# Performance work log

Hardware: AMD Instinct MI355X
Metric: run time of the kernel (lower is better)

Reference implementation:

```python
import jax, jax.numpy as jnp
import numpy as np

B, C_IN, C_OUT, H, W = 4, 256, 256, 56, 56
NH, K, P = 2, 5, 2
HD = C_OUT // NH          # 128
SE_H = C_OUT // 16        # 16
SE_H2 = max(SE_H // 16, 1)  # 1
EPS = 1e-5


def setup_inputs() -> dict:
    key = jax.random.key(0)
    ks = jax.random.split(key, 16)
    n = lambda k, sh, s=1.0: jax.random.normal(k, sh, jnp.float32) * s

    def bn_params(k, c):
        k1, k2 = jax.random.split(k)
        return (1.0 + 0.1 * n(k1, (c,)), 0.1 * n(k2, (c,)),
                jnp.zeros((c,), jnp.float32), jnp.ones((c,), jnp.float32))

    agg_g1, agg_b1, agg_m1, agg_v1 = bn_params(ks[6], C_OUT)
    agg_g2, agg_b2, agg_m2, agg_v2 = bn_params(ks[7], C_OUT)
    se_g_in, se_b_in, se_m_in, se_v_in = bn_params(ks[8], SE_H)
    se_g_out, se_b_out, se_m_out, se_v_out = bn_params(ks[9], C_OUT)
    return {
        "x": n(ks[0], (B, C_IN, H, W)),
        "Wq": n(ks[1], (C_OUT, C_IN), C_IN ** -0.5),
        "Wk": n(ks[2], (C_OUT, C_IN), C_IN ** -0.5),
        "Wv": n(ks[3], (C_OUT, C_IN), C_IN ** -0.5),
        "rel_h": n(ks[4], (HD, 1, 1, K, 1)),
        "rel_w": n(ks[5], (HD, 1, 1, 1, K)),
        "agg_g1": agg_g1, "agg_b1": agg_b1, "agg_m1": agg_m1, "agg_v1": agg_v1,
        "agg_W": n(ks[10], (C_OUT, C_OUT), C_OUT ** -0.5),
        "agg_g2": agg_g2, "agg_b2": agg_b2, "agg_m2": agg_m2, "agg_v2": agg_v2,
        "se_Win": n(ks[11], (SE_H, C_OUT), C_OUT ** -0.5),
        "se_g_in": se_g_in, "se_b_in": se_b_in, "se_m_in": se_m_in, "se_v_in": se_v_in,
        "se_fc1": n(ks[12], (SE_H2, SE_H), SE_H ** -0.5),
        "se_fc2": n(ks[13], (SE_H, SE_H2)),
        "se_Wout": n(ks[14], (C_OUT, SE_H), SE_H ** -0.5),
        "se_g_out": se_g_out, "se_b_out": se_b_out, "se_m_out": se_m_out, "se_v_out": se_v_out,
    }


def _conv1x1(Wm, t):
    return jnp.einsum('oc,bchw->bohw', Wm, t)


def _bn(t, g, b, m, v):
    # eval-mode BatchNorm2d with running stats
    return (t - m[:, None, None]) * (g * jax.lax.rsqrt(v + EPS))[:, None, None] + b[:, None, None]


def _windows(t):
    # (B, O, H+2P, W+2P) -> (B, O, H, W, K, K), matching torch unfold(2,K,1).unfold(3,K,1)
    w = jnp.stack([t[:, :, i:i + H, j:j + W] for i in range(K) for j in range(K)], axis=-1)
    return w.reshape(t.shape[0], t.shape[1], H, W, K, K)


def reference(x, Wq, Wk, Wv, rel_h, rel_w,
              agg_g1, agg_b1, agg_m1, agg_v1, agg_W, agg_g2, agg_b2, agg_m2, agg_v2,
              se_Win, se_g_in, se_b_in, se_m_in, se_v_in, se_fc1, se_fc2, se_Wout,
              se_g_out, se_b_out, se_m_out, se_v_out):
    xp = jnp.pad(x, ((0, 0), (0, 0), (P, P), (P, P)))
    q = _conv1x1(Wq, x).reshape(B, NH, HD, H, W)          # (B,NH,HD,H,W)
    k_win = _windows(_conv1x1(Wk, xp))                    # (B,O,H,W,K,K)
    v_win = _windows(_conv1x1(Wv, xp))
    # relative position bias: first head gets rel_h (height taps), second gets rel_w
    k_win = jnp.concatenate([k_win[:, :HD] + rel_h[None], k_win[:, HD:] + rel_w[None]], axis=1)
    k_r = k_win.reshape(B, NH, HD, H, W, K * K)
    v_r = v_win.reshape(B, NH, HD, H, W, K * K)
    scores = jnp.einsum('bnchw,bnchwk->bnhwk', q, k_r) / jnp.sqrt(jnp.float32(HD))
    attn = jax.nn.softmax(scores, axis=-1)
    out = jnp.einsum('bnhwk,bnchwk->bnchw', attn, v_r).reshape(B, C_OUT, H, W)
    # agg: BN -> ReLU -> 1x1 conv -> BN
    y = jax.nn.relu(_bn(out, agg_g1, agg_b1, agg_m1, agg_v1))
    y = _bn(_conv1x1(agg_W, y), agg_g2, agg_b2, agg_m2, agg_v2)
    # squeeze-excitation (intended math; original view(b,c) is a channel-count bug)
    s = jax.nn.relu(_bn(_conv1x1(se_Win, y), se_g_in, se_b_in, se_m_in, se_v_in))  # (B,SE_H,H,W)
    p = s.mean(axis=(2, 3))                                                        # (B,SE_H)
    g = jax.nn.sigmoid(jax.nn.relu(p @ se_fc1.T) @ se_fc2.T)                       # (B,SE_H)
    s = s * g[:, :, None, None]
    return _bn(_conv1x1(se_Wout, s), se_g_out, se_b_out, se_m_out, se_v_out)
```

## Files before the change

kernel.cpp:

```cpp
#include <hip/hip_runtime.h>
#include <hip/hip_bf16.h>

#define HW 3136
#define HH 56
#define WW 56
#define BB 4
#define CC 256
#define HD 128

#define TH 2
#define TW 8
#define WR 6
#define WC 12
#define WPX 72
#define KSTR2 136
#define RSTR 132

#define ASTR 72

typedef __attribute__((ext_vector_type(8))) short bf16x8;
typedef __attribute__((ext_vector_type(4))) float f32x4;

__device__ __forceinline__ unsigned short f2bf(float f) {
    unsigned int u; __builtin_memcpy(&u, &f, 4);
    unsigned int r = u + 0x7FFFu + ((u >> 16) & 1u);
    return (unsigned short)(r >> 16);
}
__device__ __forceinline__ float bflo(unsigned int u) {
    unsigned int x = u << 16; float f; __builtin_memcpy(&f, &x, 4); return f;
}
__device__ __forceinline__ float bfhi(unsigned int u) {
    unsigned int x = u & 0xFFFF0000u; float f; __builtin_memcpy(&f, &x, 4); return f;
}

__global__ __launch_bounds__(256) void xt_cvt(const float* __restrict__ x,
                                              unsigned short* __restrict__ xt)
{
    int b = blockIdx.z;
    int c0 = blockIdx.y * 64;
    int p0 = blockIdx.x * 64;
    __shared__ float tile[64][65];
    int t = threadIdx.x;
    int p4 = t & 15, cl = t >> 4;
    const float* xb = x + ((size_t)b * CC + c0) * HW + p0;
#pragma unroll
    for (int i = 0; i < 4; i++) {
        int c = cl + 16 * i;
        float4 f = *(const float4*)(xb + (size_t)c * HW + p4 * 4);
        tile[c][p4 * 4 + 0] = f.x; tile[c][p4 * 4 + 1] = f.y;
        tile[c][p4 * 4 + 2] = f.z; tile[c][p4 * 4 + 3] = f.w;
    }
    __syncthreads();
    int c2 = t & 31, pl = t >> 5;
    unsigned short* xo = xt + ((size_t)b * HW + p0) * CC + c0;
#pragma unroll
    for (int i = 0; i < 8; i++) {
        int p = pl + 8 * i;
        float a = tile[2 * c2][p], bb = tile[2 * c2 + 1][p];
        unsigned int pk = (unsigned int)f2bf(a) | ((unsigned int)f2bf(bb) << 16);
        *(unsigned int*)(xo + (size_t)p * CC + 2 * c2) = pk;
    }
}

__global__ __launch_bounds__(256) void wcvt(const float* __restrict__ Wq,
                                            const float* __restrict__ Wk,
                                            const float* __restrict__ Wv,
                                            const float* __restrict__ Wa,
                                            const float* __restrict__ Wse,
                                            unsigned short* __restrict__ wb,
                                            float* __restrict__ psum)
{
    int t = threadIdx.x;
    if (blockIdx.y == 4) {
        if (blockIdx.x == 0 && t < 64) psum[t] = 0.f;
        int idx = blockIdx.x * 256 + t;
        if (idx < 1024) {
            float4 f = *(const float4*)(Wse + (size_t)idx * 4);
            uint2 pk;
            pk.x = (unsigned int)f2bf(f.x) | ((unsigned int)f2bf(f.y) << 16);
            pk.y = (unsigned int)f2bf(f.z) | ((unsigned int)f2bf(f.w) << 16);
            *(uint2*)(wb + (size_t)4 * 65536 + (size_t)idx * 4) = pk;
        }
        return;
    }
    const float* srcs[4] = {Wq, Wk, Wv, Wa};
    const float* s = srcs[blockIdx.y];
    int idx = blockIdx.x * 256 + t;
    float4 f = *(const float4*)(s + (size_t)idx * 4);
    uint2 pk;
    pk.x = (unsigned int)f2bf(f.x) | ((unsigned int)f2bf(f.y) << 16);
    pk.y = (unsigned int)f2bf(f.z) | ((unsigned int)f2bf(f.w) << 16);
    *(uint2*)(wb + (size_t)blockIdx.y * 65536 + (size_t)idx * 4) = pk;
}

__global__ __launch_bounds__(256) void qkv_mfma(
    const unsigned short* __restrict__ xt, const unsigned short* __restrict__ wqkv,
    unsigned short* __restrict__ q_ws, unsigned short* __restrict__ k_ws,
    unsigned short* __restrict__ v_ws)
{
    int wsel = blockIdx.z;
    unsigned short* outp = (wsel == 0) ? q_ws : ((wsel == 1) ? k_ws : v_ws);
    int gp0 = blockIdx.x * 128, o0 = blockIdx.y * 128;

    __shared__ unsigned short As[128 * ASTR];
    __shared__ unsigned short Bs[128 * ASTR];
    const unsigned short* xb = xt + (size_t)gp0 * CC;
    const unsigned short* wbp = wqkv + (size_t)wsel * 65536 + (size_t)o0 * CC;

    int t = threadIdx.x;
    int wave = t >> 6, lane = t & 63;
    int mo = (wave & 1) * 64, no = (wave >> 1) * 64;
    int lm = lane & 15, lq = lane >> 4;
    int sr = t >> 3, sc = t & 7;

    f32x4 acc[4][4];
#pragma unroll
    for (int i = 0; i < 4; i++)
#pragma unroll
        for (int j = 0; j < 4; j++) acc[i][j] = (f32x4){0.f, 0.f, 0.f, 0.f};

    for (int k0 = 0; k0 < 256; k0 += 64) {
#pragma unroll
        for (int i = 0; i < 4; i++) {
            int r = sr + 32 * i;
            *(uint4*)&As[r * ASTR + sc * 8] = *(const uint4*)(xb + (size_t)r * CC + k0 + sc * 8);
            *(uint4*)&Bs[r * ASTR + sc * 8] = *(const uint4*)(wbp + (size_t)r * CC + k0 + sc * 8);
        }
        __syncthreads();
#pragma unroll
        for (int ks = 0; ks < 64; ks += 32) {
            bf16x8 af[4], bfr[4];
#pragma unroll
            for (int i = 0; i < 4; i++)
                af[i] = *(bf16x8*)&As[(mo + 16 * i + lm) * ASTR + ks + lq * 8];
#pragma unroll
            for (int j = 0; j < 4; j++)
                bfr[j] = *(bf16x8*)&Bs[(no + 16 * j + lm) * ASTR + ks + lq * 8];
#pragma unroll
            for (int i = 0; i < 4; i++)
#pragma unroll
                for (int j = 0; j < 4; j++)
                    acc[i][j] = __builtin_amdgcn_mfma_f32_16x16x32_bf16(
                        af[i], bfr[j], acc[i][j], 0, 0, 0);
        }
        __syncthreads();
    }
    unsigned short* ob = outp + (size_t)gp0 * CC + o0;
    bool ev = (lm & 1) == 0;
    int elm = lm & ~1;
#pragma unroll
    for (int i = 0; i < 4; i++)
#pragma unroll
        for (int j = 0; j < 4; j++)
#pragma unroll
            for (int r = 0; r < 4; r++) {
                float v = acc[i][j][r];
                float p = __shfl_xor(v, 1, 64);
                unsigned int pk = ev
                    ? ((unsigned int)f2bf(v) | ((unsigned int)f2bf(p) << 16))
                    : ((unsigned int)f2bf(p) | ((unsigned int)f2bf(v) << 16));
                if (ev == (r < 2)) {
                    int m = mo + 16 * i + lq * 4 + r;
                    int n = no + 16 * j + elm;
                    *(unsigned int*)(ob + (size_t)m * CC + n) = pk;
                }
            }
}

__global__ __launch_bounds__(256) void agg_mfma(
    const unsigned short* __restrict__ ao, const unsigned short* __restrict__ wagg,
    const float* __restrict__ g1, const float* __restrict__ b1,
    const float* __restrict__ m1, const float* __restrict__ v1,
    const float* __restrict__ g2, const float* __restrict__ b2,
    const float* __restrict__ m2, const float* __restrict__ v2,
    float* __restrict__ y2)
{
    int gp0 = blockIdx.x * 128, o0 = blockIdx.y * 128;

    __shared__ unsigned short As[128 * ASTR];
    __shared__ unsigned short Bs[128 * ASTR];
    __shared__ float s1[256], o1[256], s2[256], o2[256];

    int t = threadIdx.x;
    {
        float sc1 = g1[t] * rsqrtf(v1[t] + 1e-5f);
        s1[t] = sc1; o1[t] = b1[t] - m1[t] * sc1;
        float sc2 = g2[t] * rsqrtf(v2[t] + 1e-5f);
        s2[t] = sc2; o2[t] = b2[t] - m2[t] * sc2;
    }

    const unsigned short* aob = ao + (size_t)gp0 * CC;
    const unsigned short* wbp = wagg + (size_t)o0 * CC;

    int wave = t >> 6, lane = t & 63;
    int mo = (wave & 1) * 64, no = (wave >> 1) * 64;
    int lm = lane & 15, lq = lane >> 4;
    int sr = t >> 3, sc = t & 7;

    f32x4 acc[4][4];
#pragma unroll
    for (int i = 0; i < 4; i++)
#pragma unroll
        for (int j = 0; j < 4; j++) acc[i][j] = (f32x4){0.f, 0.f, 0.f, 0.f};

    __syncthreads();

    for (int k0 = 0; k0 < 256; k0 += 64) {
#pragma unroll
        for (int i = 0; i < 4; i++) {
            int r = sr + 32 * i;
            int cb = k0 + sc * 8;
            uint4 u = *(const uint4*)(aob + (size_t)r * CC + cb);
            float e[8] = {bflo(u.x), bfhi(u.x), bflo(u.y), bfhi(u.y),
                          bflo(u.z), bfhi(u.z), bflo(u.w), bfhi(u.w)};
            unsigned short pk[8];
#pragma unroll
            for (int uu = 0; uu < 8; uu++) {
                float vv = fmaxf(e[uu] * s1[cb + uu] + o1[cb + uu], 0.f);
                pk[uu] = f2bf(vv);
            }
            *(uint4*)&As[r * ASTR + sc * 8] = *(uint4*)pk;
            *(uint4*)&Bs[r * ASTR + sc * 8] = *(const uint4*)(wbp + (size_t)r * CC + k0 + sc * 8);
        }
        __syncthreads();
#pragma unroll
        for (int ks = 0; ks < 64; ks += 32) {
            bf16x8 af[4], bfr[4];
#pragma unroll
            for (int i = 0; i < 4; i++)
                af[i] = *(bf16x8*)&As[(mo + 16 * i + lm) * ASTR + ks + lq * 8];
#pragma unroll
            for (int j = 0; j < 4; j++)
                bfr[j] = *(bf16x8*)&Bs[(no + 16 * j + lm) * ASTR + ks + lq * 8];
#pragma unroll
            for (int i = 0; i < 4; i++)
#pragma unroll
                for (int j = 0; j < 4; j++)
                    acc[i][j] = __builtin_amdgcn_mfma_f32_16x16x32_bf16(
                        af[i], bfr[j], acc[i][j], 0, 0, 0);
        }
        __syncthreads();
    }
    float* yb = y2 + (size_t)gp0 * CC + o0;
#pragma unroll
    for (int i = 0; i < 4; i++)
#pragma unroll
        for (int j = 0; j < 4; j++)
#pragma unroll
            for (int r = 0; r < 4; r++) {
                int m = mo + 16 * i + lq * 4 + r;
                int n = no + 16 * j + lm;
                yb[(size_t)m * CC + n] = acc[i][j][r] * s2[o0 + n] + o2[o0 + n];
            }
}

__global__ __launch_bounds__(256) void attn_kernel(
    const unsigned short* __restrict__ q_ws, const unsigned short* __restrict__ k_ws,
    const unsigned short* __restrict__ v_ws,
    const float* __restrict__ rel_h, const float* __restrict__ rel_w,
    unsigned short* __restrict__ ao_ws)
{
    __shared__ unsigned short kwin[WPX * KSTR2];
    __shared__ float relT[5 * RSTR];

    int t = threadIdx.x;
    int tile = blockIdx.x;
    int n = blockIdx.y;
    int b = blockIdx.z;
    int tr = tile / 7, tc = tile - tr * 7;
    int h0 = tr * TH, w0 = tc * TW;
    const float* rel = (n == 0) ? rel_h : rel_w;
    const size_t base = (size_t)b * HW * CC + n * HD;

    {
        int c16 = t & 15, pwt = t >> 4;
#pragma unroll
        for (int it = 0; it < 5; it++) {
            int pw = pwt + it * 16;
            if (pw < WPX) {
                int wr = pw / 12, wc = pw - wr * 12;
                int gh = h0 + wr - 2, gw = w0 + wc - 2;
                uint4 u = make_uint4(0u, 0u, 0u, 0u);
                if (gh >= 0 && gh < HH && gw >= 0 && gw < WW)
                    u = *(const uint4*)(k_ws + base + (size_t)(gh * WW + gw) * CC + c16 * 8);
                *(uint4*)&kwin[pw * KSTR2 + c16 * 8] = u;
            }
        }
        if (t < 128) {
#pragma unroll
            for (int tt = 0; tt < 5; tt++)
                relT[tt * RSTR + t] = rel[t * 5 + tt];
        }
    }
    __syncthreads();

    int px = t >> 4, cg = t & 15;
    int pr = px >> 3, pc = px & 7;
    int ghp = h0 + pr, gwp = w0 + pc;
    const size_t pbase = base + (size_t)(ghp * WW + gwp) * CC;

    float q[8];
    {
        uint4 uq = *(const uint4*)(q_ws + pbase + cg * 8);
        q[0] = bflo(uq.x); q[1] = bfhi(uq.x); q[2] = bflo(uq.y); q[3] = bfhi(uq.y);
        q[4] = bflo(uq.z); q[5] = bfhi(uq.z); q[6] = bflo(uq.w); q[7] = bfhi(uq.w);
    }

    float acc[30];
#pragma unroll
    for (int tt = 0; tt < 25; tt++) {
        int di = tt / 5, dj = tt - 5 * (tt / 5);
        int wpx = (pr + di) * WC + pc + dj;
        uint4 ku = *(const uint4*)&kwin[wpx * KSTR2 + cg * 8];
        acc[tt] = q[0] * bflo(ku.x) + q[1] * bfhi(ku.x)
                + q[2] * bflo(ku.y) + q[3] * bfhi(ku.y)
                + q[4] * bflo(ku.z) + q[5] * bfhi(ku.z)
                + q[6] * bflo(ku.w) + q[7] * bfhi(ku.w);
    }
#pragma unroll
    for (int tt = 0; tt < 5; tt++) {
        float4 r0 = *(const float4*)&relT[tt * RSTR + cg * 8];
        float4 r1 = *(const float4*)&relT[tt * RSTR + cg * 8 + 4];
        acc[25 + tt] = q[0] * r0.x + q[1] * r0.y + q[2] * r0.z + q[3] * r0.w
                     + q[4] * r1.x + q[5] * r1.y + q[6] * r1.z + q[7] * r1.w;
    }
#pragma unroll
    for (int tt = 0; tt < 30; tt++) {
#pragma unroll
        for (int m = 1; m < 16; m <<= 1)
            acc[tt] += __shfl_xor(acc[tt], m, 64);
    }
    {
        const float inv = 0.08838834764831845f;
        float mx = -1e30f;
#pragma unroll
        for (int tt = 0; tt < 25; tt++) {
            int di = tt / 5, dj = tt - 5 * (tt / 5);
            acc[tt] = (acc[tt] + ((n == 0) ? acc[25 + di] : acc[25 + dj])) * inv;
            mx = fmaxf(mx, acc[tt]);
        }
        float sum = 0.f;
#pragma unroll
        for (int tt = 0; tt < 25; tt++) { acc[tt] = __expf(acc[tt] - mx); sum += acc[tt]; }
        float rs = 1.f / sum;
#pragma unroll
        for (int tt = 0; tt < 25; tt++) acc[tt] *= rs;
    }
    __syncthreads();

    {
        int c16 = t & 15, pwt = t >> 4;
#pragma unroll
        for (int it = 0; it < 5; it++) {
            int pw = pwt + it * 16;
            if (pw < WPX) {
                int wr = pw / 12, wc = pw - wr * 12;
                int gh = h0 + wr - 2, gw = w0 + wc - 2;
                uint4 u = make_uint4(0u, 0u, 0u, 0u);
                if (gh >= 0 && gh < HH && gw >= 0 && gw < WW)
                    u = *(const uint4*)(v_ws + base + (size_t)(gh * WW + gw) * CC + c16 * 8);
                *(uint4*)&kwin[pw * KSTR2 + c16 * 8] = u;
            }
        }
    }
    __syncthreads();

    float o[8];
#pragma unroll
    for (int i = 0; i < 8; i++) o[i] = 0.f;
#pragma unroll
    for (int tt = 0; tt < 25; tt++) {
        int di = tt / 5, dj = tt - 5 * (tt / 5);
        int wpx = (pr + di) * WC + pc + dj;
        float a = acc[tt];
        uint4 vu = *(const uint4*)&kwin[wpx * KSTR2 + cg * 8];
        o[0] += a * bflo(vu.x); o[1] += a * bfhi(vu.x);
        o[2] += a * bflo(vu.y); o[3] += a * bfhi(vu.y);
        o[4] += a * bflo(vu.z); o[5] += a * bfhi(vu.z);
        o[6] += a * bflo(vu.w); o[7] += a * bfhi(vu.w);
    }
    uint4 pk;
    pk.x = (unsigned int)f2bf(o[0]) | ((unsigned int)f2bf(o[1]) << 16);
    pk.y = (unsigned int)f2bf(o[2]) | ((unsigned int)f2bf(o[3]) << 16);
    pk.z = (unsigned int)f2bf(o[4]) | ((unsigned int)f2bf(o[5]) << 16);
    pk.w = (unsigned int)f2bf(o[6]) | ((unsigned int)f2bf(o[7]) << 16);
    *(uint4*)(ao_ws + pbase + cg * 8) = pk;
}

__global__ __launch_bounds__(256) void se_in_mfma(
    const float* __restrict__ y2, const unsigned short* __restrict__ wse,
    const float* __restrict__ gin, const float* __restrict__ bin,
    const float* __restrict__ min_, const float* __restrict__ vin,
    float* __restrict__ s_ws, float* __restrict__ psum)
{
    int wave = threadIdx.x >> 6, lane = threadIdx.x & 63;
    int tile = blockIdx.x * 4 + wave;
    int gp0 = tile * 16;
    int b = tile / 196;
    int lm = lane & 15, lq = lane >> 4;

    f32x4 acc = (f32x4){0.f, 0.f, 0.f, 0.f};
    const float* ya = y2 + (size_t)(gp0 + lm) * CC;
#pragma unroll
    for (int k0 = 0; k0 < 256; k0 += 32) {
        int kb = k0 + lq * 8;
        float4 f0 = *(const float4*)(ya + kb);
        float4 f1 = *(const float4*)(ya + kb + 4);
        unsigned short pk[8] = {f2bf(f0.x), f2bf(f0.y), f2bf(f0.z), f2bf(f0.w),
                                f2bf(f1.x), f2bf(f1.y), f2bf(f1.z), f2bf(f1.w)};
        bf16x8 af = *(bf16x8*)pk;
        bf16x8 bf = *(const bf16x8*)(wse + (size_t)lm * CC + kb);
        acc = __builtin_amdgcn_mfma_f32_16x16x32_bf16(af, bf, acc, 0, 0, 0);
    }
    float sc = gin[lm] * rsqrtf(vin[lm] + 1e-5f);
    float off = bin[lm] - min_[lm] * sc;
    float sum4 = 0.f;
#pragma unroll
    for (int r = 0; r < 4; r++) {
        int row = lq * 4 + r;
        float v = fmaxf(acc[r] * sc + off, 0.f);
        s_ws[(size_t)(gp0 + row) * 16 + lm] = v;
        sum4 += v;
    }
    sum4 += __shfl_xor(sum4, 16, 64);
    sum4 += __shfl_xor(sum4, 32, 64);
    if (lane < 16) atomicAdd(&psum[b * 16 + lane], sum4);
}

__global__ __launch_bounds__(256) void se_out_kernel(
    const float* __restrict__ s_ws, const float* __restrict__ psum,
    const float* __restrict__ fc1, const float* __restrict__ fc2,
    const float* __restrict__ se_Wout,
    const float* __restrict__ gout, const float* __restrict__ bout,
    const float* __restrict__ mout, const float* __restrict__ vout,
    float* __restrict__ out)
{
    int b = blockIdx.y;
    int px0 = blockIdx.x * 32;
    __shared__ float sl[32 * 17];
    __shared__ float wg[256 * 20];
    __shared__ float bo[256];
    __shared__ float gg[16];
    int t = threadIdx.x;

    if (t < 16) {
        float h = 0.f;
#pragma unroll
        for (int jj = 0; jj < 16; jj++)
            h += (psum[b * 16 + jj] * (1.f / 3136.f)) * fc1[jj];
        h = fmaxf(h, 0.f);
        float z = h * fc2[t];
        gg[t] = 1.f / (1.f + __expf(-z));
    }
    {
        const float* sb = s_ws + (size_t)(b * HW + px0) * 16;
#pragma unroll
        for (int i = 0; i < 2; i++) {
            int idx = t + 256 * i;
            sl[(idx >> 4) * 17 + (idx & 15)] = sb[idx];
        }
    }
    __syncthreads();
    {
        float sc = gout[t] * rsqrtf(vout[t] + 1e-5f);
        bo[t] = bout[t] - mout[t] * sc;
        const float* wr = se_Wout + (size_t)t * 16;
#pragma unroll
        for (int k = 0; k < 16; k++)
            wg[t * 20 + k] = wr[k] * gg[k] * sc;
    }
    __syncthreads();

    int px = t & 31, og = t >> 5;
    float4 s0 = *(float4*)&sl[px * 17 + 0];
    float4 s1v = *(float4*)&sl[px * 17 + 4];
    float4 s2v = *(float4*)&sl[px * 17 + 8];
    float4 s3 = *(float4*)&sl[px * 17 + 12];
    float* ob = out + (size_t)b * CC * HW + px0 + px;
#pragma unroll
    for (int oi = 0; oi < 32; oi++) {
        int o = og * 32 + oi;
        float4 w0 = *(float4*)&wg[o * 20 + 0];
        float4 w1 = *(float4*)&wg[o * 20 + 4];
        float4 w2 = *(float4*)&wg[o * 20 + 8];
        float4 w3 = *(float4*)&wg[o * 20 + 12];
        float r = bo[o]
            + s0.x * w0.x + s0.y * w0.y + s0.z * w0.z + s0.w * w0.w
            + s1v.x * w1.x + s1v.y * w1.y + s1v.z * w1.z + s1v.w * w1.w
            + s2v.x * w2.x + s2v.y * w2.y + s2v.z * w2.z + s2v.w * w2.w
            + s3.x * w3.x + s3.y * w3.y + s3.z * w3.z + s3.w * w3.w;
        ob[(size_t)o * HW] = r;
    }
}

extern "C" void kernel_launch(void* const* d_in, const int* in_sizes, int n_in,
                              void* d_out, int out_size, void* d_ws, size_t ws_size,
                              hipStream_t stream) {
    const float* x     = (const float*)d_in[0];
    const float* Wq    = (const float*)d_in[1];
    const float* Wk    = (const float*)d_in[2];
    const float* Wv    = (const float*)d_in[3];
    const float* rel_h = (const float*)d_in[4];
    const float* rel_w = (const float*)d_in[5];
    const float* agg_g1 = (const float*)d_in[6];
    const float* agg_b1 = (const float*)d_in[7];
    const float* agg_m1 = (const float*)d_in[8];
    const float* agg_v1 = (const float*)d_in[9];
    const float* agg_W  = (const float*)d_in[10];
    const float* agg_g2 = (const float*)d_in[11];
    const float* agg_b2 = (const float*)d_in[12];
    const float* agg_m2 = (const float*)d_in[13];
    const float* agg_v2 = (const float*)d_in[14];
    const float* se_Win = (const float*)d_in[15];
    const float* se_g_in = (const float*)d_in[16];
    const float* se_b_in = (const float*)d_in[17];
    const float* se_m_in = (const float*)d_in[18];
    const float* se_v_in = (const float*)d_in[19];
    const float* se_fc1  = (const float*)d_in[20];
    const float* se_fc2  = (const float*)d_in[21];
    const float* se_Wout = (const float*)d_in[22];
    const float* se_g_out = (const float*)d_in[23];
    const float* se_b_out = (const float*)d_in[24];
    const float* se_m_out = (const float*)d_in[25];
    const float* se_v_out = (const float*)d_in[26];

    const size_t NQ = (size_t)BB * HW * CC;
    unsigned short* q_ws  = (unsigned short*)d_ws;
    unsigned short* k_ws  = q_ws + NQ;
    unsigned short* v_ws  = k_ws + NQ;
    unsigned short* ao_ws = v_ws + NQ;
    unsigned short* xt    = ao_ws;
    float* y2_ws = (float*)d_ws;
    float* s_ws  = (float*)(ao_ws + NQ);
    float* psum  = s_ws + (size_t)BB * HW * 16;
    unsigned short* wbf = (unsigned short*)(psum + 64);

    xt_cvt<<<dim3(49, 4, 4), 256, 0, stream>>>(x, xt);
    wcvt<<<dim3(64, 5), 256, 0, stream>>>(Wq, Wk, Wv, agg_W, se_Win, wbf, psum);
    qkv_mfma<<<dim3(98, 2, 3), 256, 0, stream>>>(xt, wbf, q_ws, k_ws, v_ws);
    attn_kernel<<<dim3(196, 2, 4), 256, 0, stream>>>(q_ws, k_ws, v_ws, rel_h, rel_w, ao_ws);
    agg_mfma<<<dim3(98, 2), 256, 0, stream>>>(ao_ws, wbf + 3 * 65536,
        agg_g1, agg_b1, agg_m1, agg_v1, agg_g2, agg_b2, agg_m2, agg_v2, y2_ws);
    se_in_mfma<<<dim3(196), 256, 0, stream>>>(y2_ws, wbf + 4 * 65536,
        se_g_in, se_b_in, se_m_in, se_v_in, s_ws, psum);
    se_out_kernel<<<dim3(98, 4), 256, 0, stream>>>(s_ws, psum, se_fc1, se_fc2,
        se_Wout, se_g_out, se_b_out, se_m_out, se_v_out, (float*)d_out);
}
```

Measured before the change: 199.6 us.

## Drop LDS staging in attention kernel and merge prep conversion kernels

The attention kernel no longer stages a 6x12 K/V halo window in shared memory behind barriers. Each thread now reads its 25 K and V neighbours straight from global memory, relying on L1/L2 for reuse across the 16 row-contiguous pixels in a block, and reads the relative-position bias directly as well. The x transpose/convert and weight-convert kernels are merged into one launch to save a kernel launch. The risk is more global/cache traffic and less explicit reuse in attention, in exchange for removing LDS writes, syncs and the shared-memory footprint.

```diff
diff --git a/kernel.cpp b/kernel.cpp
--- a/kernel.cpp
+++ b/kernel.cpp
@@ -8,14 +8,6 @@
 #define CC 256
 #define HD 128
 
-#define TH 2
-#define TW 8
-#define WR 6
-#define WC 12
-#define WPX 72
-#define KSTR2 136
-#define RSTR 132
-
 #define ASTR 72
 
 typedef __attribute__((ext_vector_type(8))) short bf16x8;
@@ -33,36 +25,9 @@
     unsigned int x = u & 0xFFFF0000u; float f; __builtin_memcpy(&f, &x, 4); return f;
 }
 
-__global__ __launch_bounds__(256) void xt_cvt(const float* __restrict__ x,
-                                              unsigned short* __restrict__ xt)
-{
-    int b = blockIdx.z;
-    int c0 = blockIdx.y * 64;
-    int p0 = blockIdx.x * 64;
-    __shared__ float tile[64][65];
-    int t = threadIdx.x;
-    int p4 = t & 15, cl = t >> 4;
-    const float* xb = x + ((size_t)b * CC + c0) * HW + p0;
-#pragma unroll
-    for (int i = 0; i < 4; i++) {
-        int c = cl + 16 * i;
-        float4 f = *(const float4*)(xb + (size_t)c * HW + p4 * 4);
-        tile[c][p4 * 4 + 0] = f.x; tile[c][p4 * 4 + 1] = f.y;
-        tile[c][p4 * 4 + 2] = f.z; tile[c][p4 * 4 + 3] = f.w;
-    }
-    __syncthreads();
-    int c2 = t & 31, pl = t >> 5;
-    unsigned short* xo = xt + ((size_t)b * HW + p0) * CC + c0;
-#pragma unroll
-    for (int i = 0; i < 8; i++) {
-        int p = pl + 8 * i;
-        float a = tile[2 * c2][p], bb = tile[2 * c2 + 1][p];
-        unsigned int pk = (unsigned int)f2bf(a) | ((unsigned int)f2bf(bb) << 16);
-        *(unsigned int*)(xo + (size_t)p * CC + 2 * c2) = pk;
-    }
-}
-
-__global__ __launch_bounds__(256) void wcvt(const float* __restrict__ Wq,
+__global__ __launch_bounds__(256) void prep(const float* __restrict__ x,
+                                            unsigned short* __restrict__ xt,
+                                            const float* __restrict__ Wq,
                                             const float* __restrict__ Wk,
                                             const float* __restrict__ Wv,
                                             const float* __restrict__ Wa,
@@ -70,27 +35,57 @@
                                             unsigned short* __restrict__ wb,
                                             float* __restrict__ psum)
 {
+    int bid = blockIdx.x;
     int t = threadIdx.x;
-    if (blockIdx.y == 4) {
-        if (blockIdx.x == 0 && t < 64) psum[t] = 0.f;
-        int idx = blockIdx.x * 256 + t;
-        if (idx < 1024) {
-            float4 f = *(const float4*)(Wse + (size_t)idx * 4);
-            uint2 pk;
-            pk.x = (unsigned int)f2bf(f.x) | ((unsigned int)f2bf(f.y) << 16);
-            pk.y = (unsigned int)f2bf(f.z) | ((unsigned int)f2bf(f.w) << 16);
-            *(uint2*)(wb + (size_t)4 * 65536 + (size_t)idx * 4) = pk;
-        }
+    if (bid >= 784) {
+        int j = bid - 784;
+        int wy = j / 64, wx = j - wy * 64;
+        if (wy == 4) {
+            if (wx == 0 && t < 64) psum[t] = 0.f;
+            int idx = wx * 256 + t;
+            if (idx < 1024) {
+                float4 f = *(const float4*)(Wse + (size_t)idx * 4);
+                uint2 pk;
+                pk.x = (unsigned int)f2bf(f.x) | ((unsigned int)f2bf(f.y) << 16);
+                pk.y = (unsigned int)f2bf(f.z) | ((unsigned int)f2bf(f.w) << 16);
+                *(uint2*)(wb + (size_t)4 * 65536 + (size_t)idx * 4) = pk;
+            }
+            return;
+        }
+        const float* srcs[4] = {Wq, Wk, Wv, Wa};
+        const float* s = srcs[wy];
+        int idx = wx * 256 + t;
+        float4 f = *(const float4*)(s + (size_t)idx * 4);
+        uint2 pk;
+        pk.x = (unsigned int)f2bf(f.x) | ((unsigned int)f2bf(f.y) << 16);
+        pk.y = (unsigned int)f2bf(f.z) | ((unsigned int)f2bf(f.w) << 16);
+        *(uint2*)(wb + (size_t)wy * 65536 + (size_t)idx * 4) = pk;
         return;
     }
-    const float* srcs[4] = {Wq, Wk, Wv, Wa};
-    const float* s = srcs[blockIdx.y];
-    int idx = blockIdx.x * 256 + t;
-    float4 f = *(const float4*)(s + (size_t)idx * 4);
-    uint2 pk;
-    pk.x = (unsigned int)f2bf(f.x) | ((unsigned int)f2bf(f.y) << 16);
-    pk.y = (unsigned int)f2bf(f.z) | ((unsigned int)f2bf(f.w) << 16);
-    *(uint2*)(wb + (size_t)blockIdx.y * 65536 + (size_t)idx * 4) = pk;
+    int p_i = bid % 49;
+    int c_i = (bid / 49) & 3;
+    int b = bid / 196;
+    int c0 = c_i * 64, p0 = p_i * 64;
+    __shared__ float tile[64][65];
+    int p4 = t & 15, cl = t >> 4;
+    const float* xb = x + ((size_t)b * CC + c0) * HW + p0;
+#pragma unroll
+    for (int i = 0; i < 4; i++) {
+        int c = cl + 16 * i;
+        float4 f = *(const float4*)(xb + (size_t)c * HW + p4 * 4);
+        tile[c][p4 * 4 + 0] = f.x; tile[c][p4 * 4 + 1] = f.y;
+        tile[c][p4 * 4 + 2] = f.z; tile[c][p4 * 4 + 3] = f.w;
+    }
+    __syncthreads();
+    int c2 = t & 31, pl = t >> 5;
+    unsigned short* xo = xt + ((size_t)b * HW + p0) * CC + c0;
+#pragma unroll
+    for (int i = 0; i < 8; i++) {
+        int p = pl + 8 * i;
+        float a = tile[2 * c2][p], bb = tile[2 * c2 + 1][p];
+        unsigned int pk = (unsigned int)f2bf(a) | ((unsigned int)f2bf(bb) << 16);
+        *(unsigned int*)(xo + (size_t)p * CC + 2 * c2) = pk;
+    }
 }
 
 __global__ __launch_bounds__(256) void qkv_mfma(
@@ -260,75 +255,55 @@
     const float* __restrict__ rel_h, const float* __restrict__ rel_w,
     unsigned short* __restrict__ ao_ws)
 {
-    __shared__ unsigned short kwin[WPX * KSTR2];
-    __shared__ float relT[5 * RSTR];
-
     int t = threadIdx.x;
-    int tile = blockIdx.x;
-    int n = blockIdx.y;
-    int b = blockIdx.z;
-    int tr = tile / 7, tc = tile - tr * 7;
-    int h0 = tr * TH, w0 = tc * TW;
-    const float* rel = (n == 0) ? rel_h : rel_w;
+    int pxl = t >> 4, cg = t & 15;
+    int hw = blockIdx.x * 16 + pxl;
+    int n = blockIdx.y, b = blockIdx.z;
+    int h = hw / WW, w = hw - h * WW;
     const size_t base = (size_t)b * HW * CC + n * HD;
-
-    {
-        int c16 = t & 15, pwt = t >> 4;
-#pragma unroll
-        for (int it = 0; it < 5; it++) {
-            int pw = pwt + it * 16;
-            if (pw < WPX) {
-                int wr = pw / 12, wc = pw - wr * 12;
-                int gh = h0 + wr - 2, gw = w0 + wc - 2;
-                uint4 u = make_uint4(0u, 0u, 0u, 0u);
-                if (gh >= 0 && gh < HH && gw >= 0 && gw < WW)
-                    u = *(const uint4*)(k_ws + base + (size_t)(gh * WW + gw) * CC + c16 * 8);
-                *(uint4*)&kwin[pw * KSTR2 + c16 * 8] = u;
-            }
-        }
-        if (t < 128) {
-#pragma unroll
-            for (int tt = 0; tt < 5; tt++)
-                relT[tt * RSTR + t] = rel[t * 5 + tt];
-        }
-    }
-    __syncthreads();
-
-    int px = t >> 4, cg = t & 15;
-    int pr = px >> 3, pc = px & 7;
-    int ghp = h0 + pr, gwp = w0 + pc;
-    const size_t pbase = base + (size_t)(ghp * WW + gwp) * CC;
+    const size_t pbase = base + (size_t)hw * CC + cg * 8;
 
     float q[8];
     {
-        uint4 uq = *(const uint4*)(q_ws + pbase + cg * 8);
+        uint4 uq = *(const uint4*)(q_ws + pbase);
         q[0] = bflo(uq.x); q[1] = bfhi(uq.x); q[2] = bflo(uq.y); q[3] = bfhi(uq.y);
         q[4] = bflo(uq.z); q[5] = bfhi(uq.z); q[6] = bflo(uq.w); q[7] = bfhi(uq.w);
     }
 
-    float acc[30];
-#pragma unroll
-    for (int tt = 0; tt < 25; tt++) {
-        int di = tt / 5, dj = tt - 5 * (tt / 5);
-        int wpx = (pr + di) * WC + pc + dj;
-        uint4 ku = *(const uint4*)&kwin[wpx * KSTR2 + cg * 8];
-        acc[tt] = q[0] * bflo(ku.x) + q[1] * bfhi(ku.x)
+    float red[30];
+    {
+        const float* rp = ((n == 0) ? rel_h : rel_w) + cg * 40;
+#pragma unroll
+        for (int tt = 0; tt < 5; tt++) red[25 + tt] = 0.f;
+#pragma unroll
+        for (int c = 0; c < 8; c++)
+#pragma unroll
+            for (int tt = 0; tt < 5; tt++)
+                red[25 + tt] += q[c] * rp[c * 5 + tt];
+    }
+#pragma unroll
+    for (int di = 0; di < 5; di++) {
+        int hh = h + di - 2;
+        bool vr = (hh >= 0) && (hh < HH);
+        const unsigned short* krow = k_ws + base + (size_t)(hh * WW) * CC + cg * 8;
+#pragma unroll
+        for (int dj = 0; dj < 5; dj++) {
+            int ww = w + dj - 2;
+            uint4 ku = make_uint4(0u, 0u, 0u, 0u);
+            if (vr && ww >= 0 && ww < WW)
+                ku = *(const uint4*)(krow + (size_t)ww * CC);
+            red[di * 5 + dj] =
+                  q[0] * bflo(ku.x) + q[1] * bfhi(ku.x)
                 + q[2] * bflo(ku.y) + q[3] * bfhi(ku.y)
                 + q[4] * bflo(ku.z) + q[5] * bfhi(ku.z)
                 + q[6] * bflo(ku.w) + q[7] * bfhi(ku.w);
-    }
-#pragma unroll
-    for (int tt = 0; tt < 5; tt++) {
-        float4 r0 = *(const float4*)&relT[tt * RSTR + cg * 8];
-        float4 r1 = *(const float4*)&relT[tt * RSTR + cg * 8 + 4];
-        acc[25 + tt] = q[0] * r0.x + q[1] * r0.y + q[2] * r0.z + q[3] * r0.w
-                     + q[4] * r1.x + q[5] * r1.y + q[6] * r1.z + q[7] * r1.w;
+        }
     }
 #pragma unroll
     for (int tt = 0; tt < 30; tt++) {
 #pragma unroll
         for (int m = 1; m < 16; m <<= 1)
-            acc[tt] += __shfl_xor(acc[tt], m, 64);
+            red[tt] += __shfl_xor(red[tt], m, 64);
     }
     {
         const float inv = 0.08838834764831845f;
@@ -336,55 +311,43 @@
 #pragma unroll
         for (int tt = 0; tt < 25; tt++) {
             int di = tt / 5, dj = tt - 5 * (tt / 5);
-            acc[tt] = (acc[tt] + ((n == 0) ? acc[25 + di] : acc[25 + dj])) * inv;
-            mx = fmaxf(mx, acc[tt]);
+            red[tt] = (red[tt] + ((n == 0) ? red[25 + di] : red[25 + dj])) * inv;
+            mx = fmaxf(mx, red[tt]);
         }
         float sum = 0.f;
 #pragma unroll
-        for (int tt = 0; tt < 25; tt++) { acc[tt] = __expf(acc[tt] - mx); sum += acc[tt]; }
+        for (int tt = 0; tt < 25; tt++) { red[tt] = __expf(red[tt] - mx); sum += red[tt]; }
         float rs = 1.f / sum;
 #pragma unroll
-        for (int tt = 0; tt < 25; tt++) acc[tt] *= rs;
-    }
-    __syncthreads();
-
-    {
-        int c16 = t & 15, pwt = t >> 4;
-#pragma unroll
-        for (int it = 0; it < 5; it++) {
-            int pw = pwt + it * 16;
-            if (pw < WPX) {
-                int wr = pw / 12, wc = pw - wr * 12;
-                int gh = h0 + wr - 2, gw = w0 + wc - 2;
-                uint4 u = make_uint4(0u, 0u, 0u, 0u);
-                if (gh >= 0 && gh < HH && gw >= 0 && gw < WW)
-                    u = *(const uint4*)(v_ws + base + (size_t)(gh * WW + gw) * CC + c16 * 8);
-                *(uint4*)&kwin[pw * KSTR2 + c16 * 8] = u;
+        for (int tt = 0; tt < 25; tt++) red[tt] *= rs;
+    }
+    float o[8];
+#pragma unroll
+    for (int i = 0; i < 8; i++) o[i] = 0.f;
+#pragma unroll
+    for (int di = 0; di < 5; di++) {
+        int hh = h + di - 2;
+        bool vr = (hh >= 0) && (hh < HH);
+        const unsigned short* vrow = v_ws + base + (size_t)(hh * WW) * CC + cg * 8;
+#pragma unroll
+        for (int dj = 0; dj < 5; dj++) {
+            int ww = w + dj - 2;
+            if (vr && ww >= 0 && ww < WW) {
+                uint4 vu = *(const uint4*)(vrow + (size_t)ww * CC);
+                float a = red[di * 5 + dj];
+                o[0] += a * bflo(vu.x); o[1] += a * bfhi(vu.x);
+                o[2] += a * bflo(vu.y); o[3] += a * bfhi(vu.y);
+                o[4] += a * bflo(vu.z); o[5] += a * bfhi(vu.z);
+                o[6] += a * bflo(vu.w); o[7] += a * bfhi(vu.w);
             }
         }
-    }
-    __syncthreads();
-
-    float o[8];
-#pragma unroll
-    for (int i = 0; i < 8; i++) o[i] = 0.f;
-#pragma unroll
-    for (int tt = 0; tt < 25; tt++) {
-        int di = tt / 5, dj = tt - 5 * (tt / 5);
-        int wpx = (pr + di) * WC + pc + dj;
-        float a = acc[tt];
-        uint4 vu = *(const uint4*)&kwin[wpx * KSTR2 + cg * 8];
-        o[0] += a * bflo(vu.x); o[1] += a * bfhi(vu.x);
-        o[2] += a * bflo(vu.y); o[3] += a * bfhi(vu.y);
-        o[4] += a * bflo(vu.z); o[5] += a * bfhi(vu.z);
-        o[6] += a * bflo(vu.w); o[7] += a * bfhi(vu.w);
     }
     uint4 pk;
     pk.x = (unsigned int)f2bf(o[0]) | ((unsigned int)f2bf(o[1]) << 16);
     pk.y = (unsigned int)f2bf(o[2]) | ((unsigned int)f2bf(o[3]) << 16);
     pk.z = (unsigned int)f2bf(o[4]) | ((unsigned int)f2bf(o[5]) << 16);
     pk.w = (unsigned int)f2bf(o[6]) | ((unsigned int)f2bf(o[7]) << 16);
-    *(uint4*)(ao_ws + pbase + cg * 8) = pk;
+    *(uint4*)(ao_ws + pbase) = pk;
 }
 
 __global__ __launch_bounds__(256) void se_in_mfma(
@@ -535,8 +498,7 @@
     float* psum  = s_ws + (size_t)BB * HW * 16;
     unsigned short* wbf = (unsigned short*)(psum + 64);
 
-    xt_cvt<<<dim3(49, 4, 4), 256, 0, stream>>>(x, xt);
-    wcvt<<<dim3(64, 5), 256, 0, stream>>>(Wq, Wk, Wv, agg_W, se_Win, wbf, psum);
+    prep<<<dim3(1104), 256, 0, stream>>>(x, xt, Wq, Wk, Wv, agg_W, se_Win, wbf, psum);
     qkv_mfma<<<dim3(98, 2, 3), 256, 0, stream>>>(xt, wbf, q_ws, k_ws, v_ws);
     attn_kernel<<<dim3(196, 2, 4), 256, 0, stream>>>(q_ws, k_ws, v_ws, rel_h, rel_w, ao_ws);
     agg_mfma<<<dim3(98, 2), 256, 0, stream>>>(ao_ws, wbf + 3 * 65536,
```

After: 211.9 us. 6.2% more time.
